# Optimization experiments

Hardware: AMD Instinct MI355X
Metric: run time of the kernel (lower is better)

Reference implementation:

```python
import jax, jax.numpy as jnp
import numpy as np

B, L, C = 16, 2048, 1024
H, G, K = 16, 4, 5
GC = C // G          # group channels = 256
DH = C // H          # head channels = 64
PAD = K // 2         # 2


def conv1d(x, w, b, pad):
    # x: [N, Cin, L], w: [Cout, Cin, K]
    out = jax.lax.conv_general_dilated(x, w, (1,), [(pad, pad)],
                                       dimension_numbers=('NCH', 'OIH', 'NCH'))
    return out + b[None, :, None]


def setup_inputs() -> dict:
    key = jax.random.key(0)
    ks = jax.random.split(key, 16)
    s = 0.02
    inp = {
        'x': jax.random.normal(ks[0], (B, L, C), jnp.float32),
        'Wq': jax.random.normal(ks[1], (C, C), jnp.float32) * s,
        'bq': jnp.zeros((C,), jnp.float32),
        'Wk': jax.random.normal(ks[2], (C, C), jnp.float32) * s,
        'bk': jnp.zeros((C,), jnp.float32),
        'Wv': jax.random.normal(ks[3], (C, C), jnp.float32) * s,
        'bv': jnp.zeros((C,), jnp.float32),
        'Woff1': jax.random.normal(ks[4], (GC, GC, K), jnp.float32) * s,
        'boff1': jnp.zeros((GC,), jnp.float32),
        'Woff2': jax.random.normal(ks[5], (1, GC, 1), jnp.float32) * s,
        'boff2': jnp.zeros((1,), jnp.float32),
        'rpb_table': jax.random.normal(ks[6], (1, C, L), jnp.float32) * 0.02,
        'Wout': jax.random.normal(ks[7], (C, C), jnp.float32) * s,
        'bout': jnp.zeros((C,), jnp.float32),
    }
    return inp


def reference(x, Wq, bq, Wk, bk, Wv, bv, Woff1, boff1, Woff2, boff2,
              rpb_table, Wout, bout):
    xT = jnp.swapaxes(x, 1, 2)                        # [B, C, L]
    # conv1x1 q projection
    q = jnp.einsum('oc,bcl->bol', Wq, xT) + bq[None, :, None]
    gq = q.reshape(B * G, GC, L)                       # grouped queries
    # offset network: conv(k=5, pad=2) -> conv(k=1, pad=2) => length L+4
    h = conv1d(gq, Woff1, boff1, PAD)                  # [BG, GC, L]
    off = conv1d(h, Woff2, boff2, PAD)                 # [BG, 1, L+4]
    off = jnp.tanh(off[:, 0, :]) * K                   # offset_range_factor = kernel
    L4 = L + 2 * PAD
    grid = jnp.arange(L4, dtype=x.dtype)
    vgrid = grid[None, :] + off                        # [BG, L4]
    vs = 2.0 * vgrid / (L4 - 1) - 1.0                  # normalize with n = L+4 (as in source)
    # grid_sample bilinear, align_corners=False, zeros padding, over length L
    pos = ((vs + 1.0) * L - 1.0) / 2.0
    i0 = jnp.floor(pos)
    w1 = pos - i0
    i0 = i0.astype(jnp.int32)
    feats = xT.reshape(B * G, GC, L)

    def gather(idx):
        valid = ((idx >= 0) & (idx < L)).astype(x.dtype)
        idxc = jnp.clip(idx, 0, L - 1)
        g = jnp.take_along_axis(feats, jnp.broadcast_to(idxc[:, None, :], (B * G, GC, L4)), axis=2)
        return g * valid[:, None, :]

    samp = gather(i0) * (1.0 - w1)[:, None, :] + gather(i0 + 1) * w1[:, None, :]
    x_sampled = samp[:, :, :L].reshape(B, C, L)

    k = jnp.einsum('oc,bcl->bol', Wk, x_sampled) + bk[None, :, None]
    v = jnp.einsum('oc,bcl->bol', Wv, x_sampled) + bv[None, :, None] + rpb_table

    qh = q.reshape(B * H, DH, L)
    kh = k.reshape(B * H, DH, L)
    vh = v.reshape(B * H, DH, L)
    # attention over head-channel dims, contracting over sequence (faithful to source)
    scores = jnp.einsum('bil,bjl->bij', qh, kh) * (C ** -0.5)   # [BH, DH, DH]
    attn = jax.nn.softmax(scores, axis=-1)
    out = jnp.einsum('bij,bjl->bil', attn, vh)                  # [BH, DH, L]
    # rearrange '(b g) l c -> b c (g l)' with b=B, g=H, l=DH, c=L
    out = out.reshape(B, H, DH, L).transpose(0, 3, 1, 2).reshape(B, L, C)
    return out @ Wout.T + bout
```

## Files before the change

kernel.cpp:

```cpp
#include <hip/hip_runtime.h>
#include <hip/hip_bf16.h>
#include <stdint.h>

#define BATCH 16
#define SEQ   2048
#define CH    1024
#define NH    16
#define NG    4
#define KW    5
#define GCH   256
#define DHD   64
#define NBG   (BATCH*NG)
#define NBH   (BATCH*NH)
#define MROWS (BATCH*SEQ)

typedef __hip_bfloat16 bf16;
typedef float f32x4 __attribute__((ext_vector_type(4)));
typedef __bf16 bf16x8 __attribute__((ext_vector_type(8)));

__device__ __forceinline__ void unpack8(uint4 r, float* f){
    uint32_t w0=r.x,w1=r.y,w2=r.z,w3=r.w;
    f[0]=__uint_as_float(w0<<16); f[1]=__uint_as_float(w0&0xffff0000u);
    f[2]=__uint_as_float(w1<<16); f[3]=__uint_as_float(w1&0xffff0000u);
    f[4]=__uint_as_float(w2<<16); f[5]=__uint_as_float(w2&0xffff0000u);
    f[6]=__uint_as_float(w3<<16); f[7]=__uint_as_float(w3&0xffff0000u);
}

__global__ __launch_bounds__(256)
void cvt_kernel(const float* __restrict__ in, bf16* __restrict__ out, int n)
{
    int i = (blockIdx.x*256 + threadIdx.x)*8;
    if (i >= n) return;
    float4 f0 = *(const float4*)(in+i);
    float4 f1 = *(const float4*)(in+i+4);
    union { bf16 b[8]; uint4 u; } pk;
    pk.b[0]=__float2bfloat16(f0.x); pk.b[1]=__float2bfloat16(f0.y);
    pk.b[2]=__float2bfloat16(f0.z); pk.b[3]=__float2bfloat16(f0.w);
    pk.b[4]=__float2bfloat16(f1.x); pk.b[5]=__float2bfloat16(f1.y);
    pk.b[6]=__float2bfloat16(f1.z); pk.b[7]=__float2bfloat16(f1.w);
    *(uint4*)(out+i) = pk.u;
}

__global__ void prep_weff_kernel(const float* __restrict__ W1, const float* __restrict__ b1,
                                 const float* __restrict__ w2, const float* __restrict__ b2,
                                 float* __restrict__ weff, float* __restrict__ wcst)
{
    int kk = blockIdx.x;
    int cj = threadIdx.x;
    float s = 0.f;
    for (int co=0; co<GCH; ++co)
        s += w2[co] * W1[((size_t)co*GCH + cj)*KW + kk];
    weff[kk*GCH + cj] = s;
    if (kk==0 && cj==0){
        float sb = 0.f;
        for (int co=0; co<GCH; ++co) sb += w2[co]*b1[co];
        wcst[0] = b2[0];
        wcst[1] = sb;
    }
}

template<int MODE>
__global__ __launch_bounds__(512, 2)
void gemm256_kernel(const bf16* __restrict__ A, const bf16* __restrict__ Wb,
                    const float* __restrict__ bias, const float* __restrict__ rpb,
                    void* __restrict__ outp)
{
    __shared__ __bf16 SM[2*16384];
    const int t = threadIdx.x;
    const int w = t>>6, l = t&63;
    const int wrow = w>>2, wcol = w&3;
    const int lr = l&15, kq = l>>4;

    const int lin = blockIdx.x;
    const int xcd = lin&7, sblk = lin>>3;
    const int m0 = (xcd*16 + (sblk>>2))*256;
    const int n0 = (sblk&3)*256;

    const bf16* Ag = A  + (size_t)m0*CH;
    const bf16* Bg = Wb + (size_t)n0*CH;

    int srow[2], scol[2];
    #pragma unroll
    for (int r=0;r<2;++r){
        int o = (t + 512*r)*16;
        int e = o ^ (((o>>7)&3)<<4);
        srow[r] = e>>6;
        scol[r] = (e&63)>>1;
    }

    auto STAGE = [&](int tile, int buf){
        const int kt = tile*32;
        __bf16* ab = SM + buf*16384;
        __bf16* bb = ab + 8192;
        #pragma unroll
        for (int r=0;r<2;++r){
            __builtin_amdgcn_global_load_lds(
                (const __attribute__((address_space(1))) void*)(Ag + (size_t)srow[r]*CH + kt + scol[r]),
                (__attribute__((address_space(3))) void*)(ab + w*512 + r*4096), 16, 0, 0);
            __builtin_amdgcn_global_load_lds(
                (const __attribute__((address_space(1))) void*)(Bg + (size_t)srow[r]*CH + kt + scol[r]),
                (__attribute__((address_space(3))) void*)(bb + w*512 + r*4096), 16, 0, 0);
        }
    };

    f32x4 acc[8][4];
    #pragma unroll
    for (int i=0;i<8;++i)
        #pragma unroll
        for (int j=0;j<4;++j) acc[i][j] = (f32x4){0.f,0.f,0.f,0.f};

    STAGE(0, 0);
    asm volatile("s_waitcnt vmcnt(0)" ::: "memory");
    __builtin_amdgcn_s_barrier();

    const int NT = CH/32;
    for (int tt=0; tt<NT; ++tt){
        const int cur = tt&1;
        if (tt+1 < NT) STAGE(tt+1, cur^1);
        __builtin_amdgcn_sched_barrier(0);

        const __bf16* As_ = SM + cur*16384;
        const __bf16* Bs_ = As_ + 8192;
        bf16x8 af[8], bfr[4];
        #pragma unroll
        for (int fi=0; fi<8; ++fi){
            int row = wrow*128 + fi*16 + lr;
            int o = row*64 + kq*16;
            o ^= ((o>>7)&3)<<4;
            af[fi] = *(const bf16x8*)(As_ + (o>>1));
        }
        #pragma unroll
        for (int fj=0; fj<4; ++fj){
            int row = wcol*64 + fj*16 + lr;
            int o = row*64 + kq*16;
            o ^= ((o>>7)&3)<<4;
            bfr[fj] = *(const bf16x8*)(Bs_ + (o>>1));
        }
        #pragma unroll
        for (int fi=0; fi<8; ++fi)
            #pragma unroll
            for (int fj=0; fj<4; ++fj)
                acc[fi][fj] = __builtin_amdgcn_mfma_f32_16x16x32_bf16(af[fi], bfr[fj], acc[fi][fj], 0,0,0);

        asm volatile("s_waitcnt lgkmcnt(0)" ::: "memory");
        asm volatile("s_waitcnt vmcnt(0)" ::: "memory");
        __builtin_amdgcn_s_barrier();
    }

    float bs[4];
    #pragma unroll
    for (int fj=0;fj<4;++fj) bs[fj] = bias[n0 + wcol*64 + fj*16 + lr];

    if constexpr (MODE == 2){
        const int bb2 = m0 >> 11;
        const int l0g = m0 & (SEQ-1);
        bf16* outT = (bf16*)outp;
        #pragma unroll
        for (int fi=0; fi<8; ++fi){
            int rowl = wrow*128 + fi*16 + kq*4;
            #pragma unroll
            for (int fj=0; fj<4; ++fj){
                int col = n0 + wcol*64 + fj*16 + lr;
                union { bf16 h[4]; uint2 u; } pk;
                #pragma unroll
                for (int r=0;r<4;++r) pk.h[r] = __float2bfloat16(acc[fi][fj][r] + bs[fj]);
                *(uint2*)(outT + ((size_t)(bb2*CH + col))*SEQ + l0g + rowl) = pk.u;
            }
        }
    } else {
        #pragma unroll
        for (int fi=0; fi<8; ++fi){
            #pragma unroll
            for (int r=0;r<4;++r){
                int mg = m0 + wrow*128 + fi*16 + kq*4 + r;
                int lseq = mg & (SEQ-1);
                #pragma unroll
                for (int fj=0; fj<4; ++fj){
                    int ng = n0 + wcol*64 + fj*16 + lr;
                    float v = acc[fi][fj][r] + bs[fj];
                    if constexpr (MODE==1) v += rpb[(size_t)ng*SEQ + lseq];
                    if constexpr (MODE==3)
                        ((float*)outp)[(size_t)mg*CH + ng] = v;
                    else
                        ((bf16*)outp)[(size_t)mg*CH + ng] = __float2bfloat16(v);
                }
            }
        }
    }
}

__global__ __launch_bounds__(256)
void offsets_kernel(const bf16* __restrict__ QT, const float* __restrict__ weff,
                    const float* __restrict__ wcst, float* __restrict__ posb)
{
    __shared__ float P5R[8][272][5];
    __shared__ float weffL[KW][GCH];
    const int t = threadIdx.x;
    const int chunk = blockIdx.x, bg = blockIdx.y;
    const int b = bg>>2, g = bg&3;
    const int l0 = chunk*256;

    for (int i = t; i < KW*GCH; i += 256) weffL[i>>8][i&255] = weff[i];
    __syncthreads();

    const int jg = t & 31, cg = t >> 5;

    auto doblock = [&](int jb, int cgx){
        const int j0 = l0 - 8 + jb*8;
        float acc[8][KW];
        #pragma unroll
        for (int e=0;e<8;++e)
            #pragma unroll
            for (int kk=0;kk<KW;++kk) acc[e][kk] = 0.f;
        const bf16* base = QT + ((size_t)(b*CH + g*GCH + cgx*32))*SEQ;
        const bool safe = (j0 >= 0) && (j0 + 8 <= SEQ);
        if (safe){
            #pragma unroll 4
            for (int i=0;i<32;++i){
                float xv[8];
                { union { bf16x8 v; uint4 u; } cv;
                  cv.v = *(const bf16x8*)(base + (size_t)i*SEQ + j0);
                  unpack8(cv.u, xv); }
                float wk[KW];
                #pragma unroll
                for (int kk=0;kk<KW;++kk) wk[kk] = weffL[kk][cgx*32 + i];
                #pragma unroll
                for (int e=0;e<8;++e)
                    #pragma unroll
                    for (int kk=0;kk<KW;++kk) acc[e][kk] += xv[e]*wk[kk];
            }
        } else {
            for (int i=0;i<32;++i){
                float wk[KW];
                #pragma unroll
                for (int kk=0;kk<KW;++kk) wk[kk] = weffL[kk][cgx*32 + i];
                #pragma unroll
                for (int e=0;e<8;++e){
                    int j = j0 + e;
                    float xv = (j >= 0 && j < SEQ)
                             ? __bfloat162float(base[(size_t)i*SEQ + j]) : 0.f;
                    #pragma unroll
                    for (int kk=0;kk<KW;++kk) acc[e][kk] += xv*wk[kk];
                }
            }
        }
        #pragma unroll
        for (int e=0;e<8;++e)
            #pragma unroll
            for (int kk=0;kk<KW;++kk) P5R[cgx][jb*8+e][kk] = acc[e][kk];
    };

    doblock(jg, cg);
    if (t < 16) doblock(32 + (t&1), t>>1);
    __syncthreads();

    const int lp = l0 + t;
    const float b2 = wcst[0], wb1 = wcst[1];
    float o;
    if (lp < 2){
        o = b2;
    } else {
        float s = b2 + wb1;
        #pragma unroll
        for (int kk=0;kk<KW;++kk){
            int j = lp - 4 + kk;
            if (j >= 0 && j < SEQ){
                int jp = t + 4 + kk;
                float v = 0.f;
                #pragma unroll
                for (int c8=0;c8<8;++c8) v += P5R[c8][jp][kk];
                s += v;
            }
        }
        o = s;
    }
    float off = tanhf(o) * (float)KW;
    posb[bg*SEQ + lp] = ((float)lp + off) * (2048.0f/2051.0f) - 0.5f;
}

__global__ __launch_bounds__(256)
void sample_kernel(const bf16* __restrict__ Xbf, const float* __restrict__ posb,
                   bf16* __restrict__ XS)
{
    const int ci = threadIdx.x, bg = blockIdx.y;
    const int b = bg>>2, g = bg&3;
    const int lp0 = blockIdx.x*8;
    #pragma unroll
    for (int s8=0; s8<8; ++s8){
        int lp = lp0 + s8;
        float p  = posb[bg*SEQ + lp];
        float fl = floorf(p);
        float w1 = p - fl;
        int i0 = (int)fl;
        float v = 0.f;
        if (i0 >= 0 && i0 < SEQ)
            v += __bfloat162float(Xbf[((size_t)(b*SEQ + i0))*CH + g*GCH + ci]) * (1.f - w1);
        if (i0+1 >= 0 && i0+1 < SEQ)
            v += __bfloat162float(Xbf[((size_t)(b*SEQ + i0 + 1))*CH + g*GCH + ci]) * w1;
        XS[((size_t)(b*SEQ + lp))*CH + g*GCH + ci] = __float2bfloat16(v);
    }
}

__global__ __launch_bounds__(256)
void attn_fused_kernel(const bf16* __restrict__ QT, const bf16* __restrict__ KT,
                       const bf16* __restrict__ V, bf16* __restrict__ F)
{
    __shared__ float Sc[64][69];
    __shared__ float red[64][4];
    __shared__ float mrow[64];
    __shared__ float sinv[64];
    __shared__ __bf16 Pl[64][72];
    const int t = threadIdx.x, w = t>>6, l = t&63;
    const int bh = blockIdx.x, b = bh>>4, h = bh&15;
    const bf16* q = QT + ((size_t)(b*CH + h*DHD))*SEQ;
    const bf16* k = KT + ((size_t)(b*CH + h*DHD))*SEQ;
    const int lr = l&15, lk = (l>>4)*8;

    f32x4 acc[4][4];
    #pragma unroll
    for (int i=0;i<4;++i)
        #pragma unroll
        for (int j=0;j<4;++j) acc[i][j] = (f32x4){0.f,0.f,0.f,0.f};

    for (int ks=0; ks<16; ++ks){
        int kp = w*512 + ks*32 + lk;
        bf16x8 af[4], bk8[4];
        #pragma unroll
        for (int i=0;i<4;++i) af[i]  = *(const bf16x8*)(q + (size_t)(i*16+lr)*SEQ + kp);
        #pragma unroll
        for (int j=0;j<4;++j) bk8[j] = *(const bf16x8*)(k + (size_t)(j*16+lr)*SEQ + kp);
        #pragma unroll
        for (int i=0;i<4;++i)
            #pragma unroll
            for (int j=0;j<4;++j)
                acc[i][j] = __builtin_amdgcn_mfma_f32_16x16x32_bf16(af[i], bk8[j], acc[i][j], 0,0,0);
    }
    for (int wv=0; wv<4; ++wv){
        if (w == wv){
            #pragma unroll
            for (int i=0;i<4;++i)
                #pragma unroll
                for (int j=0;j<4;++j)
                    #pragma unroll
                    for (int r=0;r<4;++r){
                        int m = i*16 + (l>>4)*4 + r, n = j*16 + lr;
                        if (wv==0) Sc[m][n]  = acc[i][j][r];
                        else       Sc[m][n] += acc[i][j][r];
                    }
        }
        __syncthreads();
    }
    const int r0 = t & 63, p = t >> 6;
    const float SCALE = 0.03125f;
    float mx = -1e30f;
    #pragma unroll
    for (int c=0;c<16;++c) mx = fmaxf(mx, Sc[r0][p*16+c]*SCALE);
    red[r0][p] = mx;
    __syncthreads();
    if (t < 64) mrow[t] = fmaxf(fmaxf(red[t][0],red[t][1]), fmaxf(red[t][2],red[t][3]));
    __syncthreads();
    float m = mrow[r0], s = 0.f;
    #pragma unroll
    for (int c=0;c<16;++c){
        float e = expf(Sc[r0][p*16+c]*SCALE - m);
        Sc[r0][p*16+c] = e;
        s += e;
    }
    red[r0][p] = s;
    __syncthreads();
    if (t < 64) sinv[t] = 1.f/(red[t][0]+red[t][1]+red[t][2]+red[t][3]);
    __syncthreads();
    float inv = sinv[r0];
    #pragma unroll
    for (int e=0;e<16;++e)
        Pl[r0][p*16+e] = (__bf16)__float2bfloat16(Sc[r0][p*16+e]*inv);
    __syncthreads();

    const size_t base = (size_t)b*SEQ*CH + (size_t)h*DHD;
    bf16x8 pf[4][2];
    #pragma unroll
    for (int ks=0; ks<2; ++ks)
        #pragma unroll
        for (int ni=0;ni<4;++ni)
            pf[ni][ks] = *(const bf16x8*)&Pl[ni*16+lr][ks*32+lk];

    for (int c8=0; c8<8; ++c8){
        const int lw = c8*256 + w*64;
        f32x4 po[4][4];
        #pragma unroll
        for (int i=0;i<4;++i)
            #pragma unroll
            for (int j=0;j<4;++j) po[i][j] = (f32x4){0.f,0.f,0.f,0.f};
        #pragma unroll
        for (int ks=0; ks<2; ++ks){
            bf16x8 vf[4];
            #pragma unroll
            for (int mi=0;mi<4;++mi)
                vf[mi] = *(const bf16x8*)(V + base + (size_t)(lw + mi*16 + lr)*CH + ks*32 + lk);
            #pragma unroll
            for (int mi=0;mi<4;++mi)
                #pragma unroll
                for (int ni=0;ni<4;++ni)
                    po[mi][ni] = __builtin_amdgcn_mfma_f32_16x16x32_bf16(vf[mi], pf[ni][ks], po[mi][ni], 0,0,0);
        }
        #pragma unroll
        for (int mi=0;mi<4;++mi){
            #pragma unroll
            for (int r=0;r<4;++r){
                int lpos = lw + mi*16 + (l>>4)*4 + r;
                #pragma unroll
                for (int ni=0;ni<4;++ni)
                    F[base + (size_t)lpos*CH + ni*16 + lr] =
                        __float2bfloat16(po[mi][ni][r]);
            }
        }
    }
}

extern "C" void kernel_launch(void* const* d_in, const int* in_sizes, int n_in,
                              void* d_out, int out_size, void* d_ws, size_t ws_size,
                              hipStream_t stream)
{
    const float* x   = (const float*)d_in[0];
    const float* Wq  = (const float*)d_in[1];
    const float* bq  = (const float*)d_in[2];
    const float* Wk  = (const float*)d_in[3];
    const float* bk  = (const float*)d_in[4];
    const float* Wv  = (const float*)d_in[5];
    const float* bv  = (const float*)d_in[6];
    const float* W1  = (const float*)d_in[7];
    const float* b1  = (const float*)d_in[8];
    const float* w2  = (const float*)d_in[9];
    const float* b2  = (const float*)d_in[10];
    const float* rpb = (const float*)d_in[11];
    const float* Wo  = (const float*)d_in[12];
    const float* bo  = (const float*)d_in[13];

    char* ws = (char*)d_ws;
    bf16*  Xbf  = (bf16*)(ws);
    bf16*  QT   = (bf16*)(ws + (size_t) 67108864);
    bf16*  XS   = (bf16*)(ws + (size_t)134217728);
    bf16*  VB   = (bf16*)(ws + (size_t)201326592);
    bf16*  wslot= (bf16*)(ws + (size_t)270532608);
    float* posb = (float*)(ws + (size_t)272629760);
    float* weff = (float*)(ws + (size_t)273154048);
    float* wcst = (float*)(ws + (size_t)273159168);
    bf16*  KT = Xbf;
    bf16*  Fb = XS;

    prep_weff_kernel<<<dim3(KW), dim3(GCH), 0, stream>>>(W1, b1, w2, b2, weff, wcst);
    cvt_kernel<<<dim3(MROWS*CH/8/256), 256, 0, stream>>>(x, Xbf, MROWS*CH);

    cvt_kernel<<<dim3(CH*CH/8/256), 256, 0, stream>>>(Wq, wslot, CH*CH);
    gemm256_kernel<2><<<dim3(512), 512, 0, stream>>>(Xbf, wslot, bq, nullptr, QT);

    offsets_kernel<<<dim3(SEQ/256, NBG), 256, 0, stream>>>(QT, weff, wcst, posb);
    sample_kernel<<<dim3(SEQ/8, NBG), 256, 0, stream>>>(Xbf, posb, XS);

    cvt_kernel<<<dim3(CH*CH/8/256), 256, 0, stream>>>(Wk, wslot, CH*CH);
    gemm256_kernel<2><<<dim3(512), 512, 0, stream>>>(XS, wslot, bk, nullptr, KT);

    cvt_kernel<<<dim3(CH*CH/8/256), 256, 0, stream>>>(Wv, wslot, CH*CH);
    gemm256_kernel<1><<<dim3(512), 512, 0, stream>>>(XS, wslot, bv, rpb, VB);

    attn_fused_kernel<<<dim3(NBH), 256, 0, stream>>>(QT, KT, VB, Fb);

    cvt_kernel<<<dim3(CH*CH/8/256), 256, 0, stream>>>(Wo, wslot, CH*CH);
    gemm256_kernel<3><<<dim3(512), 512, 0, stream>>>(Fb, wslot, bo, nullptr, (float*)d_out);
}
```

Before: 625.1 us.

## Triple-buffer GEMM LDS with register ping-pong fragments and MFMA priority

```diff
diff --git a/kernel.cpp b/kernel.cpp
--- a/kernel.cpp
+++ b/kernel.cpp
@@ -61,11 +61,11 @@
 
 template<int MODE>
 __global__ __launch_bounds__(512, 2)
-void gemm256_kernel(const bf16* __restrict__ A, const bf16* __restrict__ Wb,
+void gemm_rp_kernel(const bf16* __restrict__ A, const bf16* __restrict__ Wb,
                     const float* __restrict__ bias, const float* __restrict__ rpb,
                     void* __restrict__ outp)
 {
-    __shared__ __bf16 SM[2*16384];
+    __shared__ __bf16 SM[3*16384];
     const int t = threadIdx.x;
     const int w = t>>6, l = t&63;
     const int wrow = w>>2, wcol = w&3;
@@ -103,6 +103,41 @@
         }
     };
 
+    bf16x8 afP[8], bfP[4], afQ[8], bfQ[4];
+
+    auto READ_P = [&](int buf){
+        const __bf16* As_ = SM + buf*16384;
+        const __bf16* Bs_ = As_ + 8192;
+        #pragma unroll
+        for (int fi=0; fi<8; ++fi){
+            int o = (wrow*128 + fi*16 + lr)*64 + kq*16;
+            o ^= ((o>>7)&3)<<4;
+            afP[fi] = *(const bf16x8*)(As_ + (o>>1));
+        }
+        #pragma unroll
+        for (int fj=0; fj<4; ++fj){
+            int o = (wcol*64 + fj*16 + lr)*64 + kq*16;
+            o ^= ((o>>7)&3)<<4;
+            bfP[fj] = *(const bf16x8*)(Bs_ + (o>>1));
+        }
+    };
+    auto READ_Q = [&](int buf){
+        const __bf16* As_ = SM + buf*16384;
+        const __bf16* Bs_ = As_ + 8192;
+        #pragma unroll
+        for (int fi=0; fi<8; ++fi){
+            int o = (wrow*128 + fi*16 + lr)*64 + kq*16;
+            o ^= ((o>>7)&3)<<4;
+            afQ[fi] = *(const bf16x8*)(As_ + (o>>1));
+        }
+        #pragma unroll
+        for (int fj=0; fj<4; ++fj){
+            int o = (wcol*64 + fj*16 + lr)*64 + kq*16;
+            o ^= ((o>>7)&3)<<4;
+            bfQ[fj] = *(const bf16x8*)(Bs_ + (o>>1));
+        }
+    };
+
     f32x4 acc[8][4];
     #pragma unroll
     for (int i=0;i<8;++i)
@@ -110,41 +145,48 @@
         for (int j=0;j<4;++j) acc[i][j] = (f32x4){0.f,0.f,0.f,0.f};
 
     STAGE(0, 0);
-    asm volatile("s_waitcnt vmcnt(0)" ::: "memory");
+    STAGE(1, 1);
+    asm volatile("s_waitcnt vmcnt(4)" ::: "memory");
     __builtin_amdgcn_s_barrier();
+    READ_P(0);
+    asm volatile("s_waitcnt lgkmcnt(0)" ::: "memory");
+    __builtin_amdgcn_sched_barrier(0);
 
     const int NT = CH/32;
-    for (int tt=0; tt<NT; ++tt){
-        const int cur = tt&1;
-        if (tt+1 < NT) STAGE(tt+1, cur^1);
+    for (int tt=0; tt<NT; tt+=2){
+        if (tt+2 < NT) STAGE(tt+2, (tt+2)%3);
+        if (tt+2 < NT) asm volatile("s_waitcnt vmcnt(4)" ::: "memory");
+        else           asm volatile("s_waitcnt vmcnt(0)" ::: "memory");
+        __builtin_amdgcn_s_barrier();
+        READ_Q((tt+1)%3);
         __builtin_amdgcn_sched_barrier(0);
-
-        const __bf16* As_ = SM + cur*16384;
-        const __bf16* Bs_ = As_ + 8192;
-        bf16x8 af[8], bfr[4];
-        #pragma unroll
-        for (int fi=0; fi<8; ++fi){
-            int row = wrow*128 + fi*16 + lr;
-            int o = row*64 + kq*16;
-            o ^= ((o>>7)&3)<<4;
-            af[fi] = *(const bf16x8*)(As_ + (o>>1));
-        }
-        #pragma unroll
-        for (int fj=0; fj<4; ++fj){
-            int row = wcol*64 + fj*16 + lr;
-            int o = row*64 + kq*16;
-            o ^= ((o>>7)&3)<<4;
-            bfr[fj] = *(const bf16x8*)(Bs_ + (o>>1));
-        }
+        __builtin_amdgcn_s_setprio(1);
         #pragma unroll
         for (int fi=0; fi<8; ++fi)
             #pragma unroll
             for (int fj=0; fj<4; ++fj)
-                acc[fi][fj] = __builtin_amdgcn_mfma_f32_16x16x32_bf16(af[fi], bfr[fj], acc[fi][fj], 0,0,0);
-
+                acc[fi][fj] = __builtin_amdgcn_mfma_f32_16x16x32_bf16(afP[fi], bfP[fj], acc[fi][fj], 0,0,0);
+        __builtin_amdgcn_s_setprio(0);
         asm volatile("s_waitcnt lgkmcnt(0)" ::: "memory");
-        asm volatile("s_waitcnt vmcnt(0)" ::: "memory");
         __builtin_amdgcn_s_barrier();
+        __builtin_amdgcn_sched_barrier(0);
+
+        if (tt+3 < NT) STAGE(tt+3, (tt+3)%3);
+        if (tt+3 < NT) asm volatile("s_waitcnt vmcnt(4)" ::: "memory");
+        else           asm volatile("s_waitcnt vmcnt(0)" ::: "memory");
+        __builtin_amdgcn_s_barrier();
+        if (tt+2 < NT) READ_P((tt+2)%3);
+        __builtin_amdgcn_sched_barrier(0);
+        __builtin_amdgcn_s_setprio(1);
+        #pragma unroll
+        for (int fi=0; fi<8; ++fi)
+            #pragma unroll
+            for (int fj=0; fj<4; ++fj)
+                acc[fi][fj] = __builtin_amdgcn_mfma_f32_16x16x32_bf16(afQ[fi], bfQ[fj], acc[fi][fj], 0,0,0);
+        __builtin_amdgcn_s_setprio(0);
+        asm volatile("s_waitcnt lgkmcnt(0)" ::: "memory");
+        __builtin_amdgcn_s_barrier();
+        __builtin_amdgcn_sched_barrier(0);
     }
 
     float bs[4];
@@ -452,19 +494,19 @@
     cvt_kernel<<<dim3(MROWS*CH/8/256), 256, 0, stream>>>(x, Xbf, MROWS*CH);
 
     cvt_kernel<<<dim3(CH*CH/8/256), 256, 0, stream>>>(Wq, wslot, CH*CH);
-    gemm256_kernel<2><<<dim3(512), 512, 0, stream>>>(Xbf, wslot, bq, nullptr, QT);
+    gemm_rp_kernel<2><<<dim3(512), 512, 0, stream>>>(Xbf, wslot, bq, nullptr, QT);
 
     offsets_kernel<<<dim3(SEQ/256, NBG), 256, 0, stream>>>(QT, weff, wcst, posb);
     sample_kernel<<<dim3(SEQ/8, NBG), 256, 0, stream>>>(Xbf, posb, XS);
 
     cvt_kernel<<<dim3(CH*CH/8/256), 256, 0, stream>>>(Wk, wslot, CH*CH);
-    gemm256_kernel<2><<<dim3(512), 512, 0, stream>>>(XS, wslot, bk, nullptr, KT);
+    gemm_rp_kernel<2><<<dim3(512), 512, 0, stream>>>(XS, wslot, bk, nullptr, KT);
 
     cvt_kernel<<<dim3(CH*CH/8/256), 256, 0, stream>>>(Wv, wslot, CH*CH);
-    gemm256_kernel<1><<<dim3(512), 512, 0, stream>>>(XS, wslot, bv, rpb, VB);
+    gemm_rp_kernel<1><<<dim3(512), 512, 0, stream>>>(XS, wslot, bv, rpb, VB);
 
     attn_fused_kernel<<<dim3(NBH), 256, 0, stream>>>(QT, KT, VB, Fb);
 
     cvt_kernel<<<dim3(CH*CH/8/256), 256, 0, stream>>>(Wo, wslot, CH*CH);
-    gemm256_kernel<3><<<dim3(512), 512, 0, stream>>>(Fb, wslot, bo, nullptr, (float*)d_out);
-}
+    gemm_rp_kernel<3><<<dim3(512), 512, 0, stream>>>(Fb, wslot, bo, nullptr, (float*)d_out);
+}
```

Measured after the change: 639.4 us. 2.3% more time.
